# Optimization experiments

Measured on AMD Instinct MI355X. Metric: run time of the kernel, lower is better.

## Reference

```python
import jax, jax.numpy as jnp
import numpy as np

MAX_DISP = 4          # displacement radius -> 9x9 = 81 output channels
B, C, H, W = 8, 128, 96, 160


def setup_inputs() -> dict:
    key = jax.random.key(0)
    k1, k2 = jax.random.split(key)
    tensorFirst = jax.random.normal(k1, (B, C, H, W), dtype=jnp.float32)
    tensorSecond = jax.random.normal(k2, (B, C, H, W), dtype=jnp.float32)
    return {"tensorFirst": tensorFirst, "tensorSecond": tensorSecond}


def correlation(first, second):
    # first, second: [B, C, H, W]
    b, c, h, w = first.shape
    d = MAX_DISP
    pad = jnp.pad(second, ((0, 0), (0, 0), (d, d), (d, d)))  # [B,C,H+8,W+8]
    inv_c = jnp.asarray(1.0 / c, dtype=first.dtype)
    # channel order: (dy+4)*9 + (dx+4), dx fastest (matches CUDA kernel)
    chans = [
        (first * pad[:, :, dy:dy + h, dx:dx + w]).sum(axis=1) * inv_c
        for dy in range(2 * d + 1)
        for dx in range(2 * d + 1)
    ]
    return jnp.stack(chans, axis=1)  # [B, 81, H, W]


def reference(tensorFirst, tensorSecond):
    return correlation(tensorFirst, tensorSecond)
```

## Files before the change

### kernel.cpp

```cpp
#include <hip/hip_runtime.h>
#include <stdint.h>


typedef __attribute__((ext_vector_type(8))) short bf16x8;
typedef __attribute__((ext_vector_type(4))) float f32x4;

constexpr int Bn = 8, Cn = 128, Hn = 96, Wn = 160;
constexpr int CHS = Hn * Wn;
constexpr int YP  = Hn + 8;
constexpr int XPD = Wn + 16;
constexpr size_t SECP_OCTS  = (size_t)Bn * 16 * YP * XPD;
constexpr size_t SECP_BYTES = SECP_OCTS * 16;

__device__ __forceinline__ uint32_t bf16rne(float f) {
    uint32_t u = __float_as_uint(f);
    return (u + 0x7FFFu + ((u >> 16) & 1u)) >> 16;
}
__device__ __forceinline__ uint32_t pk(float a, float b) {
    return bf16rne(a) | (bf16rne(b) << 16);
}

__global__ __launch_bounds__(256)
void prepass(const float* __restrict__ sec, uint4* __restrict__ secp)
{
    const int idx = blockIdx.x * 256 + threadIdx.x;
    const int xp  = idx % XPD;
    const int t1  = idx / XPD;
    const int yp  = t1 % YP;
    const int t2  = t1 / YP;
    const int oc  = t2 & 15;
    const int b   = t2 >> 4;
    const int y = yp - 4, x = xp - 8;
    uint4 o = make_uint4(0u, 0u, 0u, 0u);
    if (y >= 0 && y < Hn && x >= 0 && x < Wn) {
        const float* src = sec + ((size_t)b * Cn + 8 * oc) * CHS + (size_t)y * Wn + x;
        float f[8];
        #pragma unroll
        for (int j = 0; j < 8; ++j) f[j] = src[(size_t)j * CHS];
        o.x = pk(f[0], f[1]); o.y = pk(f[2], f[3]);
        o.z = pk(f[4], f[5]); o.w = pk(f[6], f[7]);
    }
    secp[idx] = o;
}

__global__ __launch_bounds__(256, 4)
void corrmain(const float* __restrict__ first, const uint4* __restrict__ secp,
              float* __restrict__ out)
{
    __shared__ float sm[4 * 1952];

    const int tid  = threadIdx.x;
    const int w    = tid >> 6;
    const int lane = tid & 63;
    const int quad = lane >> 4;
    const int n16  = lane & 15;
    const int s    = w & 1;
    const int rp   = w >> 1;

    const int d    = (int)blockIdx.x + 10 * ((int)blockIdx.y + 24 * (int)blockIdx.z);
    const int tile = (d & 7) * 240 + (d >> 3);
    const int b    = tile / 240;
    const int rem  = tile % 240;
    const int y0   = (rem / 10) * 4;
    const int x0   = (rem % 10) * 16;

    const uint4* sb = secp
        + ((size_t)(b * 16 + quad) * YP + (y0 + 2 * rp)) * XPD
        + x0 + 8 * s + 4 + n16;

    uint4 cur[10];
    #pragma unroll
    for (int zi = 0; zi < 10; ++zi) cur[zi] = sb[(size_t)zi * XPD];

    bf16x8 aF[4];
    {
        const float* fp = first + (size_t)b * Cn * CHS
                        + (size_t)(y0 + 2 * rp + (n16 >> 3)) * Wn
                        + x0 + 8 * s + (n16 & 7);
        #pragma unroll
        for (int kc = 0; kc < 4; ++kc) {
            float f[8];
            #pragma unroll
            for (int j = 0; j < 8; ++j)
                f[j] = fp[(size_t)(32 * kc + 8 * quad + j) * CHS];
            union { uint32_t u[4]; bf16x8 v; } cv;
            cv.u[0] = pk(f[0], f[1]); cv.u[1] = pk(f[2], f[3]);
            cv.u[2] = pk(f[4], f[5]); cv.u[3] = pk(f[6], f[7]);
            aF[kc] = cv.v;
        }
    }

    f32x4 acc[10];
    #pragma unroll
    for (int zi = 0; zi < 10; ++zi) acc[zi] = (f32x4){0.f, 0.f, 0.f, 0.f};

    #pragma unroll
    for (int kc = 0; kc < 4; ++kc) {
        #pragma unroll
        for (int zi = 0; zi < 10; ++zi) {
            union { uint4 u; bf16x8 v; } bf;
            bf.u = cur[zi];
            if (kc < 3)
                cur[zi] = sb[(size_t)((kc + 1) * 4 * YP + zi) * XPD];
            acc[zi] = __builtin_amdgcn_mfma_f32_16x16x32_bf16(
                          aF[kc], bf.v, acc[zi], 0, 0, 0);
        }
    }

    const float inv = 1.0f / 128.0f;
    const int wb = w * 1952;
    #pragma unroll
    for (int zi = 0; zi < 10; ++zi)
        #pragma unroll
        for (int reg = 0; reg < 4; ++reg) {
            const int rh  = quad >> 1;
            const int px  = (quad & 1) * 4 + reg;
            const int dyc = zi - rh;
            const int dxc = n16 - px;
            if (dyc >= 0 && dyc <= 8 && dxc >= 0 && dxc <= 8)
                sm[wb + ((rh * 81) + dyc * 9 + dxc) * 12 + px] = acc[zi][reg] * inv;
        }
    __syncthreads();
    float* ob = out + (size_t)b * 81 * CHS + (size_t)(y0 + 2 * rp) * Wn + x0 + 8 * s;
    #pragma unroll
    for (int ii = 0; ii < 6; ++ii) {
        int slot = lane + ii * 64;
        if (slot < 324) {
            int rh  = (slot >= 162) ? 1 : 0;
            int rm  = slot - 162 * rh;
            int c   = rm >> 1, g = rm & 1;
            float4 v = *(const float4*)&sm[wb + (rh * 81 + c) * 12 + 4 * g];
            *(float4*)(ob + (size_t)c * CHS + (size_t)rh * Wn + 4 * g) = v;
        }
    }
}

__global__ __launch_bounds__(512, 4)
void corrfb(const float* __restrict__ first, const float* __restrict__ second,
            float* __restrict__ out)
{
    __shared__ uint4 smem[16 * 32 * 4];

    const int tid  = threadIdx.x;
    const int w    = tid >> 6;
    const int lane = tid & 63;
    const int quad = lane >> 4;
    const int n16  = lane & 15;
    const int r    = w;

    const int d    = (int)blockIdx.x + 10 * ((int)blockIdx.y + 12 * (int)blockIdx.z);
    const int tile = (d & 7) * 120 + (d >> 3);
    const int b    = tile / 120;
    const int rem  = tile % 120;
    const int y0   = (rem / 10) * 8;
    const int x0   = (rem % 10) * 16;
    const int y    = y0 + r;

    const float* sb = second + (size_t)b * Cn * CHS;
    int goff[4], lpos[4];
    bool val[4];
    #pragma unroll
    for (int i = 0; i < 4; ++i) {
        int e   = tid + i * 512;
        int row = e >> 7;
        int xw  = (e >> 2) & 31;
        int q   = e & 3;
        int gy  = y0 + row - 4, gx = x0 + xw - 8;
        val[i]  = (gy >= 0) && (gy < Hn) && (gx >= 0) && (gx < Wn);
        goff[i] = val[i] ? (8 * q * CHS + gy * Wn + gx) : 0;
        lpos[i] = (row * 32 + xw) * 4 + ((q + xw + (xw >> 2)) & 3);
    }

    int bo[2];
    #pragma unroll
    for (int t = 0; t < 2; ++t) {
        int xwr = 16 * t + n16;
        bo[t] = xwr * 4 + ((quad + xwr + (xwr >> 2)) & 3);
    }

    const float* fp = first + (size_t)b * Cn * CHS + (size_t)y * Wn + x0 + n16;

    f32x4 acc[9][2];
    #pragma unroll
    for (int dy = 0; dy < 9; ++dy)
        #pragma unroll
        for (int t = 0; t < 2; ++t)
            acc[dy][t] = (f32x4){0.f, 0.f, 0.f, 0.f};

    float f0[2][8];
    #pragma unroll
    for (int i = 0; i < 2; ++i)
        #pragma unroll
        for (int j = 0; j < 8; ++j)
            f0[i][j] = sb[goff[i] + (size_t)j * CHS];

    #pragma unroll
    for (int kc = 0; kc < 4; ++kc) {
        #pragma unroll
        for (int i = 0; i < 2; ++i) {
            uint4 o;
            o.x = pk(f0[i][0], f0[i][1]); o.y = pk(f0[i][2], f0[i][3]);
            o.z = pk(f0[i][4], f0[i][5]); o.w = pk(f0[i][6], f0[i][7]);
            if (!val[i]) o = make_uint4(0u, 0u, 0u, 0u);
            smem[lpos[i]] = o;
        }
        float f1[2][8], fa[8];
        #pragma unroll
        for (int i = 0; i < 2; ++i)
            #pragma unroll
            for (int j = 0; j < 8; ++j)
                f1[i][j] = sb[goff[2 + i] + (size_t)(32 * kc + j) * CHS];
        #pragma unroll
        for (int j = 0; j < 8; ++j)
            fa[j] = fp[(size_t)(32 * kc + 8 * quad + j) * CHS];
        #pragma unroll
        for (int i = 0; i < 2; ++i) {
            uint4 o;
            o.x = pk(f1[i][0], f1[i][1]); o.y = pk(f1[i][2], f1[i][3]);
            o.z = pk(f1[i][4], f1[i][5]); o.w = pk(f1[i][6], f1[i][7]);
            if (!val[2 + i]) o = make_uint4(0u, 0u, 0u, 0u);
            smem[lpos[2 + i]] = o;
        }
        bf16x8 aF;
        {
            union { uint32_t u[4]; bf16x8 v; } cv;
            cv.u[0] = pk(fa[0], fa[1]); cv.u[1] = pk(fa[2], fa[3]);
            cv.u[2] = pk(fa[4], fa[5]); cv.u[3] = pk(fa[6], fa[7]);
            aF = cv.v;
        }
        __syncthreads();
        if (kc < 3) {
            #pragma unroll
            for (int i = 0; i < 2; ++i)
                #pragma unroll
                for (int j = 0; j < 8; ++j)
                    f0[i][j] = sb[goff[i] + (size_t)(32 * (kc + 1) + j) * CHS];
        }
        #pragma unroll
        for (int dy = 0; dy < 9; ++dy) {
            const int rb = (r + dy) * 128;
            #pragma unroll
            for (int t = 0; t < 2; ++t) {
                union { uint4 u; bf16x8 v; } bf;
                bf.u = smem[rb + bo[t]];
                acc[dy][t] = __builtin_amdgcn_mfma_f32_16x16x32_bf16(
                                 aF, bf.v, acc[dy][t], 0, 0, 0);
            }
        }
        __syncthreads();
    }

    const float inv = 1.0f / 128.0f;
    float* sm = (float*)smem;
    float* ob = out + (size_t)b * 81 * CHS + (size_t)y * Wn + x0;
    const int wb = w * 540;
    #pragma unroll
    for (int ck = 0; ck < 3; ++ck) {
        #pragma unroll
        for (int dd = 0; dd < 3; ++dd)
            #pragma unroll
            for (int t = 0; t < 2; ++t)
                #pragma unroll
                for (int reg = 0; reg < 4; ++reg) {
                    int mm  = quad * 4 + reg;
                    int dxc = 16 * t + n16 - mm - 4;
                    if (dxc >= 0 && dxc <= 8)
                        sm[wb + (dd * 9 + dxc) * 20 + mm] = acc[ck * 3 + dd][t][reg] * inv;
                }
        __syncthreads();
        #pragma unroll
        for (int ii = 0; ii < 2; ++ii) {
            int slot = lane + ii * 64;
            if (slot < 108) {
                int chn = slot >> 2, g = slot & 3;
                float4 v = *(const float4*)&sm[wb + chn * 20 + 4 * g];
                int ch = (ck * 3 + chn / 9) * 9 + chn % 9;
                *(float4*)(ob + (size_t)ch * CHS + 4 * g) = v;
            }
        }
        __syncthreads();
    }
}

extern "C" void kernel_launch(void* const* d_in, const int* in_sizes, int n_in,
                              void* d_out, int out_size, void* d_ws, size_t ws_size,
                              hipStream_t stream) {
    (void)in_sizes; (void)n_in; (void)out_size;
    const float* first  = (const float*)d_in[0];
    const float* second = (const float*)d_in[1];
    float* out = (float*)d_out;

    if (ws_size >= SECP_BYTES) {
        uint4* secp = (uint4*)d_ws;
        prepass<<<dim3((unsigned)(SECP_OCTS / 256), 1, 1), dim3(256, 1, 1), 0, stream>>>(
            second, secp);
        corrmain<<<dim3(10, 24, 8), dim3(256, 1, 1), 0, stream>>>(first, secp, out);
    } else {
        corrfb<<<dim3(Wn / 16, Hn / 8, Bn), dim3(512, 1, 1), 0, stream>>>(
            first, second, out);
    }
}
```

Baseline: 190.7 us.

## Stage second-tensor tiles in LDS via async global_load_lds with double buffering

Blocks now cover 8 rows instead of 4, with 512 threads each. The padded bf16 second-tensor window for each channel chunk is loaded cooperatively into LDS using global_load_lds, double-buffered across the four K chunks. Before, each wave loaded its own overlapping rows straight into registers, so the same data was fetched from global memory several times. The new scheme aims to cut that redundant traffic and register pressure, at the cost of a barrier per chunk, a large 62 KB LDS footprint and lower block occupancy.

After: 177.7 us. 6.8% less time.

```diff
diff --git a/kernel.cpp b/kernel.cpp
--- a/kernel.cpp
+++ b/kernel.cpp
@@ -43,11 +43,13 @@
     secp[idx] = o;
 }
 
-__global__ __launch_bounds__(256, 4)
+__global__ __launch_bounds__(512, 4)
 void corrmain(const float* __restrict__ first, const uint4* __restrict__ secp,
               float* __restrict__ out)
 {
-    __shared__ float sm[4 * 1952];
+    __shared__ __align__(16) char smemRaw[62464];
+    uint4* smemS = (uint4*)smemRaw;
+    float* smE   = (float*)smemRaw;
 
     const int tid  = threadIdx.x;
     const int w    = tid >> 6;
@@ -57,35 +59,48 @@
     const int s    = w & 1;
     const int rp   = w >> 1;
 
-    const int d    = (int)blockIdx.x + 10 * ((int)blockIdx.y + 24 * (int)blockIdx.z);
-    const int tile = (d & 7) * 240 + (d >> 3);
-    const int b    = tile / 240;
-    const int rem  = tile % 240;
-    const int y0   = (rem / 10) * 4;
+    const int d    = (int)blockIdx.x + 10 * ((int)blockIdx.y + 12 * (int)blockIdx.z);
+    const int tile = (d & 7) * 120 + (d >> 3);
+    const int b    = tile / 120;
+    const int rem  = tile % 120;
+    const int y0   = (rem / 10) * 8;
     const int x0   = (rem % 10) * 16;
 
-    const uint4* sb = secp
-        + ((size_t)(b * 16 + quad) * YP + (y0 + 2 * rp)) * XPD
-        + x0 + 8 * s + 4 + n16;
-
-    uint4 cur[10];
-    #pragma unroll
-    for (int zi = 0; zi < 10; ++zi) cur[zi] = sb[(size_t)zi * XPD];
+    size_t gsl[3];
+    #pragma unroll
+    for (int i = 0; i < 3; ++i) {
+        int sig = i * 512 + tid;
+        int q   = sig / 384;
+        int rm  = sig % 384;
+        int row = rm / 24;
+        int xw  = rm % 24;
+        gsl[i] = ((size_t)(b * 16 + q) * YP + (y0 + row)) * XPD + (x0 + 4 + xw);
+    }
+    const size_t kstep = (size_t)4 * YP * XPD;
+
+    #pragma unroll
+    for (int i = 0; i < 3; ++i)
+        __builtin_amdgcn_global_load_lds(
+            (const uint32_t*)(secp + gsl[i]),
+            (uint32_t*)(smemS + i * 512 + w * 64),
+            16, 0, 0);
 
     bf16x8 aF[4];
     {
         const float* fp = first + (size_t)b * Cn * CHS
                         + (size_t)(y0 + 2 * rp + (n16 >> 3)) * Wn
                         + x0 + 8 * s + (n16 & 7);
+        float fA[4][8];
+        #pragma unroll
+        for (int kc = 0; kc < 4; ++kc)
+            #pragma unroll
+            for (int j = 0; j < 8; ++j)
+                fA[kc][j] = fp[(size_t)(32 * kc + 8 * quad + j) * CHS];
         #pragma unroll
         for (int kc = 0; kc < 4; ++kc) {
-            float f[8];
-            #pragma unroll
-            for (int j = 0; j < 8; ++j)
-                f[j] = fp[(size_t)(32 * kc + 8 * quad + j) * CHS];
             union { uint32_t u[4]; bf16x8 v; } cv;
-            cv.u[0] = pk(f[0], f[1]); cv.u[1] = pk(f[2], f[3]);
-            cv.u[2] = pk(f[4], f[5]); cv.u[3] = pk(f[6], f[7]);
+            cv.u[0] = pk(fA[kc][0], fA[kc][1]); cv.u[1] = pk(fA[kc][2], fA[kc][3]);
+            cv.u[2] = pk(fA[kc][4], fA[kc][5]); cv.u[3] = pk(fA[kc][6], fA[kc][7]);
             aF[kc] = cv.v;
         }
     }
@@ -94,17 +109,28 @@
     #pragma unroll
     for (int zi = 0; zi < 10; ++zi) acc[zi] = (f32x4){0.f, 0.f, 0.f, 0.f};
 
+    __syncthreads();
+
     #pragma unroll
     for (int kc = 0; kc < 4; ++kc) {
+        if (kc < 3) {
+            const int nb = (kc + 1) & 1;
+            #pragma unroll
+            for (int i = 0; i < 3; ++i)
+                __builtin_amdgcn_global_load_lds(
+                    (const uint32_t*)(secp + gsl[i] + kstep * (kc + 1)),
+                    (uint32_t*)(smemS + nb * 1536 + i * 512 + w * 64),
+                    16, 0, 0);
+        }
+        const int cb = (kc & 1) * 1536;
         #pragma unroll
         for (int zi = 0; zi < 10; ++zi) {
             union { uint4 u; bf16x8 v; } bf;
-            bf.u = cur[zi];
-            if (kc < 3)
-                cur[zi] = sb[(size_t)((kc + 1) * 4 * YP + zi) * XPD];
+            bf.u = smemS[cb + quad * 384 + (2 * rp + zi) * 24 + 8 * s + n16];
             acc[zi] = __builtin_amdgcn_mfma_f32_16x16x32_bf16(
                           aF[kc], bf.v, acc[zi], 0, 0, 0);
         }
+        __syncthreads();
     }
 
     const float inv = 1.0f / 128.0f;
@@ -118,7 +144,7 @@
             const int dyc = zi - rh;
             const int dxc = n16 - px;
             if (dyc >= 0 && dyc <= 8 && dxc >= 0 && dxc <= 8)
-                sm[wb + ((rh * 81) + dyc * 9 + dxc) * 12 + px] = acc[zi][reg] * inv;
+                smE[wb + ((rh * 81) + dyc * 9 + dxc) * 12 + px] = acc[zi][reg] * inv;
         }
     __syncthreads();
     float* ob = out + (size_t)b * 81 * CHS + (size_t)(y0 + 2 * rp) * Wn + x0 + 8 * s;
@@ -127,9 +153,9 @@
         int slot = lane + ii * 64;
         if (slot < 324) {
             int rh  = (slot >= 162) ? 1 : 0;
-            int rm  = slot - 162 * rh;
-            int c   = rm >> 1, g = rm & 1;
-            float4 v = *(const float4*)&sm[wb + (rh * 81 + c) * 12 + 4 * g];
+            int rm2 = slot - 162 * rh;
+            int c   = rm2 >> 1, g = rm2 & 1;
+            float4 v = *(const float4*)&smE[wb + (rh * 81 + c) * 12 + 4 * g];
             *(float4*)(ob + (size_t)c * CHS + (size_t)rh * Wn + 4 * g) = v;
         }
     }
@@ -294,7 +320,7 @@
         uint4* secp = (uint4*)d_ws;
         prepass<<<dim3((unsigned)(SECP_OCTS / 256), 1, 1), dim3(256, 1, 1), 0, stream>>>(
             second, secp);
-        corrmain<<<dim3(10, 24, 8), dim3(256, 1, 1), 0, stream>>>(first, secp, out);
+        corrmain<<<dim3(10, 12, 8), dim3(512, 1, 1), 0, stream>>>(first, secp, out);
     } else {
         corrfb<<<dim3(Wn / 16, Hn / 8, Bn), dim3(512, 1, 1), 0, stream>>>(
             first, second, out);
```
